# Optimization experiments

Measured on AMD Instinct MI355X. Metric: run time of the kernel, lower is better.

Reference implementation:

```python
import math
import jax, jax.numpy as jnp
import numpy as np

Bn, NA, NE = 16384, 15, 16
H, NH, DH = 256, 4, 64
DO, DA, DE = 30, 32, 32
NACT, BS = 6, 2048


def setup_inputs():
    key = jax.random.key(0)
    c = [0]
    def nxt():
        c[0] += 1
        return jax.random.fold_in(key, c[0])
    def nrm(shape, scale=1.0):
        return jax.random.normal(nxt(), shape, jnp.float32) * scale
    sH = 1.0 / math.sqrt(H)
    own_raw = nrm((Bn, 1, DO))
    ally_raw = nrm((Bn, NA, DA))
    enemy_raw = nrm((Bn, NE, DE))
    # zero-rows encode invisible entities (mask is derived from all-zero check)
    mA = jax.random.bernoulli(nxt(), 0.8, (Bn, NA)).at[:, 0].set(True)
    mE = jax.random.bernoulli(nxt(), 0.8, (Bn, NE)).at[:, 0].set(True)
    ally_raw = ally_raw * mA[..., None]
    enemy_raw = enemy_raw * mE[..., None]
    return dict(
        own_raw=own_raw, ally_raw=ally_raw, enemy_raw=enemy_raw,
        hidden_state=nrm((Bn, H), 0.1),
        W_own=nrm((H, DO), 1.0 / math.sqrt(DO)), b_own=jnp.zeros((H,)),
        W_ally=nrm((H, DA), 1.0 / math.sqrt(DA)), b_ally=jnp.zeros((H,)),
        W_enemy=nrm((H, DE), 1.0 / math.sqrt(DE)), b_enemy=jnp.zeros((H,)),
        gt_w=nrm((2,), 0.1), gt_b=jnp.zeros((2,)),
        attnA_W=nrm((4, H, H), sH), attnA_b=jnp.zeros((4, H)),
        attnE_W=nrm((4, H, H), sH), attnE_b=jnp.zeros((4, H)),
        clnA_W=nrm((2, H, H), 0.1 * sH), clnA_b=jnp.zeros((2, H)),
        clnE_W=nrm((2, H, H), 0.1 * sH), clnE_b=jnp.zeros((2, H)),
        ln3_g=jnp.ones((3 * H,)), ln3_b=jnp.zeros((3 * H,)),
        gru_Wih=nrm((3 * H, 3 * H), 1.0 / math.sqrt(3 * H)),
        gru_Whh=nrm((3 * H, H), sH),
        gru_bih=jnp.zeros((3 * H,)), gru_bhh=jnp.zeros((3 * H,)),
        Wv_head=nrm((1, H), sH), bv_head=jnp.zeros((1,)),
        Wtb=nrm((2, H), sH), btb=jnp.zeros((2,)),
        log_tau=jnp.zeros((2,)),
        Wmq=nrm((H, H), sH), bmq=jnp.zeros((H,)),
        prototypes=nrm((NACT, H), sH),
        Wqs=nrm((H, H), sH), bqs=jnp.zeros((H,)),
        Wke=nrm((H, H), sH), bke=jnp.zeros((H,)),
        bs=BS,
    )


def _group_temp(cnt, w, b):
    # GroupTemp: positive temperature from group cardinality
    return jax.nn.softplus(w * jnp.log1p(cnt) + b) + 1.0


def _mhga(q, K, mask, temp, W, b):
    # multi-head group attention: single query over a small entity set
    B, N, _ = K.shape
    qh = (q @ W[0].T + b[0]).reshape(B, NH, DH)
    kh = (K @ W[1].T + b[1]).reshape(B, N, NH, DH)
    vh = (K @ W[2].T + b[2]).reshape(B, N, NH, DH)
    s = jnp.einsum('bhd,bnhd->bhn', qh, kh) / math.sqrt(DH)
    s = s / temp[:, None, None]
    s = jnp.where(mask[:, None, :], s, -1e30)
    p = jax.nn.softmax(s, axis=-1)
    z = jnp.einsum('bhn,bnhd->bhd', p, vh).reshape(B, H)
    return z @ W[3].T + b[3]


def _cln(x, cond, W, b, eps=1e-5):
    # conditional LayerNorm: scale/shift predicted from own-feature embedding
    mu = x.mean(-1, keepdims=True)
    var = ((x - mu) ** 2).mean(-1, keepdims=True)
    xn = (x - mu) * jax.lax.rsqrt(var + eps)
    gamma = 1.0 + cond @ W[0].T + b[0]
    beta = cond @ W[1].T + b[1]
    return gamma * xn + beta


def _ln(x, g, b, eps=1e-5):
    mu = x.mean(-1, keepdims=True)
    var = ((x - mu) ** 2).mean(-1, keepdims=True)
    return (x - mu) * jax.lax.rsqrt(var + eps) * g + b


def reference(own_raw, ally_raw, enemy_raw, hidden_state, W_own, b_own,
              W_ally, b_ally, W_enemy, b_enemy, gt_w, gt_b,
              attnA_W, attnA_b, attnE_W, attnE_b,
              clnA_W, clnA_b, clnE_W, clnE_b, ln3_g, ln3_b,
              gru_Wih, gru_Whh, gru_bih, gru_bhh,
              Wv_head, bv_head, Wtb, btb, log_tau,
              Wmq, bmq, prototypes, Wqs, bqs, Wke, bke, bs):
    ally_mask = jnp.any(ally_raw != 0, axis=-1)     # [B,nA]
    enemy_mask = jnp.any(enemy_raw != 0, axis=-1)   # [B,nE]
    e_own = own_raw @ W_own.T + b_own               # [B,1,H]
    A = ally_raw @ W_ally.T + b_ally                # [B,nA,H]
    E = enemy_raw @ W_enemy.T + b_enemy             # [B,nE,H]
    q_src = e_own[:, 0]
    tA = _group_temp(ally_mask.sum(-1).astype(jnp.float32), gt_w[0], gt_b[0])
    tE = _group_temp(enemy_mask.sum(-1).astype(jnp.float32), gt_w[1], gt_b[1])
    zA = _cln(_mhga(q_src, A, ally_mask, tA, attnA_W, attnA_b), q_src, clnA_W, clnA_b)
    zE = _cln(_mhga(q_src, E, enemy_mask, tE, attnE_W, attnE_b), q_src, clnE_W, clnE_b)
    u = _ln(jnp.concatenate([q_src, zA, zE], axis=-1), ln3_g, ln3_b)
    # GRUCell (PyTorch gate layout: r, z, n)
    gi = u @ gru_Wih.T + gru_bih
    gh = hidden_state @ gru_Whh.T + gru_bhh
    ir, iz, inn = jnp.split(gi, 3, axis=-1)
    hr, hz, hn = jnp.split(gh, 3, axis=-1)
    r = jax.nn.sigmoid(ir + hr)
    zg = jax.nn.sigmoid(iz + hz)
    n = jnp.tanh(inn + r * hn)
    h = (1.0 - zg) * n + zg * hidden_state
    V = h @ Wv_head.T + bv_head                     # [B,1]
    tb = h @ Wtb.T + btb
    b_move, b_shoot = tb[:, 0:1], tb[:, 1:2]
    tau_move = jnp.exp(log_tau[0]) + 1e-6
    tau_shoot = jnp.exp(log_tau[1]) + 1e-6
    # prototype movement head
    q_mv = h @ Wmq.T + bmq
    A_move = q_mv @ prototypes.T / math.sqrt(H)
    A_move = A_move - A_move.mean(-1, keepdims=True)
    Q_move = V + b_move + A_move / tau_move
    # shoot pointer head over enemies
    q_sh = h @ Wqs.T + bqs
    Ke = E @ Wke.T + bke
    a = jnp.einsum('bh,bnh->bn', q_sh, Ke) / math.sqrt(H)
    emf = enemy_mask.astype(a.dtype)
    den = jnp.maximum(emf.sum(1, keepdims=True), 1.0)
    a = a - (a * emf).sum(1, keepdims=True) / den
    a = jnp.where(enemy_mask, a, -1e30)
    Q_shoot = V + b_shoot + a / tau_shoot
    Q = jnp.concatenate([Q_move, Q_shoot], axis=-1)[:, None, :]  # [B,1,NACT+nE]
    return Q, h.reshape(bs, -1, H)
```

## Files before the change

kernel.cpp:

```cpp
#include <hip/hip_runtime.h>
#include <math.h>

#define BN 16384

typedef float f32x4 __attribute__((ext_vector_type(4)));
typedef short bf16x8v __attribute__((ext_vector_type(8)));
typedef unsigned short u16x8 __attribute__((ext_vector_type(8)));
typedef unsigned short u16x4 __attribute__((ext_vector_type(4)));

static __device__ inline unsigned short f2bf(float f) {
  unsigned u = __float_as_uint(f);
  return (unsigned short)((u + 0x8000u) >> 16);
}
static __device__ inline float bf2f(unsigned short u) {
  return __uint_as_float(((unsigned)u) << 16);
}

#define WKA_OFF   0
#define WVA_OFF   8192
#define WKE_OFF   16384
#define WVE_OFF   24576
#define WKEF_OFF  32768
#define BKA_OFF   40960
#define BVA_OFF   41216
#define BKE_OFF   41472
#define BVE_OFF   41728
#define BKEF_OFF  41984
#define WMP_OFF   43008
#define BMP_OFF   44544
#define G_OFF     45056
#define BG_OFF    53248
#define WQB_OFF   53312
#define SC0_OFF   53568
#define BMG_OFF   53632
#define CLB_OFF   53888
#define BPJA_OFF  57088
#define BPJE_OFF  57344
#define BGRU_OFF  57600
#define BHD_OFF   16384

#define QSRC_OFF  65536
#define BUF1_OFF  (QSRC_OFF + BN*256)
#define BUF2_OFF  (BUF1_OFF + BN*256)
#define BUF3_OFF  (BUF2_OFF + BN*256)
#define BUF4_OFF  (BUF3_OFF + BN*256)
#define BUF5_OFF  (BUF4_OFF + BN*256)

#define GBUF_OFF  BUF1_OFF
#define AOUTA_OFF BUF3_OFF
#define AOUTE_OFF BUF4_OFF
#define GBB_OFF   BUF5_OFF
#define UB_OFF    (BUF5_OFF + 8388608)

#define HOFF      (BN*22)

#define MGB_S 0
#define CLA_S 65536
#define CLE_S 196608
#define PJA_S 327680
#define PJE_S 360448

__global__ __launch_bounds__(256) void k_fuseA(
    const float* __restrict__ attnA_W, const float* __restrict__ attnA_b,
    const float* __restrict__ attnE_W, const float* __restrict__ attnE_b,
    const float* __restrict__ W_ally,  const float* __restrict__ b_ally,
    const float* __restrict__ W_enemy, const float* __restrict__ b_enemy,
    const float* __restrict__ Wke,     const float* __restrict__ bke,
    const float* __restrict__ clnA_W,  const float* __restrict__ clnE_W,
    float* __restrict__ FW, unsigned short* __restrict__ WBc) {
  int g = blockIdx.x * 256 + threadIdx.x;
  if (g < 40960) {
    int m = g >> 13;
    int r = g & 8191;
    int d = r >> 5, j = r & 31;
    const float *Wout, *Win, *bin, *bout; float *dst, *dstb;
    switch (m) {
      case 0: Wout = attnA_W + 65536;  Win = W_ally;  bin = b_ally;  bout = attnA_b + 256; dst = FW + WKA_OFF;  dstb = FW + BKA_OFF;  break;
      case 1: Wout = attnA_W + 131072; Win = W_ally;  bin = b_ally;  bout = attnA_b + 512; dst = FW + WVA_OFF;  dstb = FW + BVA_OFF;  break;
      case 2: Wout = attnE_W + 65536;  Win = W_enemy; bin = b_enemy; bout = attnE_b + 256; dst = FW + WKE_OFF;  dstb = FW + BKE_OFF;  break;
      case 3: Wout = attnE_W + 131072; Win = W_enemy; bin = b_enemy; bout = attnE_b + 512; dst = FW + WVE_OFF;  dstb = FW + BVE_OFF;  break;
      default:Wout = Wke;              Win = W_enemy; bin = b_enemy; bout = bke;           dst = FW + WKEF_OFF; dstb = FW + BKEF_OFF; break;
    }
    float acc = 0.f;
    for (int c = 0; c < 256; ++c) acc += Wout[d*256 + c] * Win[c*32 + j];
    dst[d*32 + j] = acc;
    if (j == 0) {
      float b = bout[d];
      for (int c = 0; c < 256; ++c) b += Wout[d*256 + c] * bin[c];
      dstb[d] = b;
    }
  } else {
    int t = g - 40960;
    if (t < 65536) {
      int e = t * 4;
      const float* src = (e < 131072) ? clnA_W : clnE_W;
      int off = (e < 131072) ? 0 : 131072;
      float4 v = *(const float4*)(src + (e - off));
      u16x4 b; b.x = f2bf(v.x); b.y = f2bf(v.y); b.z = f2bf(v.z); b.w = f2bf(v.w);
      *(u16x4*)&WBc[CLA_S + e] = b;
    }
  }
}

__global__ __launch_bounds__(256) void k_fuseB(
    const float* __restrict__ protos, const float* __restrict__ Wmq,
    const float* __restrict__ bmq,    const float* __restrict__ Wqs,
    const float* __restrict__ bqs,
    const float* __restrict__ attnA_W, const float* __restrict__ attnA_b,
    const float* __restrict__ attnE_W, const float* __restrict__ attnE_b,
    const float* __restrict__ clnA_b,  const float* __restrict__ clnE_b,
    float* __restrict__ FW, unsigned short* __restrict__ WBc) {
  int g = blockIdx.x * 256 + threadIdx.x;
  const float* WKe_f = FW + WKEF_OFF;
  const float* bKe_f = FW + BKEF_OFF;
  if (g < 10240) {
    if (g < 1536) {
      int i = g >> 8, c = g & 255;
      float acc = 0.f;
      for (int d = 0; d < 256; ++d) acc += protos[i*256 + d] * Wmq[d*256 + c];
      FW[WMP_OFF + i*256 + c] = acc;
    } else if (g < 9728) {
      int r = g - 1536;
      int j = r >> 8, c = r & 255;
      float acc = 0.f;
      for (int d = 0; d < 256; ++d) acc += WKe_f[d*32 + j] * Wqs[d*256 + c];
      FW[G_OFF + j*256 + c] = acc;
    } else if (g < 9984) {
      int c = g - 9728;
      float acc = 0.f;
      for (int d = 0; d < 256; ++d) acc += Wqs[d*256 + c] * bKe_f[d];
      FW[WQB_OFF + c] = acc;
    } else if (g < 9990) {
      int i = g - 9984;
      float acc = 0.f;
      for (int d = 0; d < 256; ++d) acc += protos[i*256 + d] * bmq[d];
      FW[BMP_OFF + i] = acc;
    } else if (g < 10022) {
      int j = g - 9990;
      float acc = 0.f;
      for (int d = 0; d < 256; ++d) acc += WKe_f[d*32 + j] * bqs[d];
      FW[BG_OFF + j] = acc;
    } else if (g == 10022) {
      float acc = 0.f;
      for (int d = 0; d < 256; ++d) acc += bqs[d] * bKe_f[d];
      FW[SC0_OFF] = acc;
    }
  } else if (g < 77056) {
    int t = g - 10240;
    if (t < 65536) {
      int r = t >> 8, c = t & 255;
      int br = r >> 7, jj = r & 127, h = jj >> 5, jc = jj & 31;
      const float* W0 = br ? attnE_W : attnA_W;
      const float* Wk = FW + (br ? WKE_OFF : WKA_OFF);
      float acc = 0.f;
      for (int d = 0; d < 64; ++d)
        acc += W0[(h*64+d)*256 + c] * Wk[(h*64+d)*32 + jc];
      WBc[MGB_S + r*256 + c] = f2bf(acc);
    } else if (t < 65792) {
      int r = t - 65536;
      int br = r >> 7, jj = r & 127, h = jj >> 5, jc = jj & 31;
      const float* b0 = br ? attnE_b : attnA_b;
      const float* Wk = FW + (br ? WKE_OFF : WKA_OFF);
      float acc = 0.f;
      for (int d = 0; d < 64; ++d) acc += b0[h*64+d] * Wk[(h*64+d)*32 + jc];
      FW[BMG_OFF + r] = acc;
    } else {
      int c = t - 65792;
      FW[CLB_OFF + c] = (c < 512) ? clnA_b[c] : clnE_b[c - 512];
    }
  } else {
    int t = g - 77056;
    if (t < 65536) {
      int br = t >> 15;
      int r0 = t & 32767;
      int o = r0 >> 7, r = r0 & 127, h = r >> 5, j = r & 31;
      const float* Wp = (br ? attnE_W : attnA_W) + 196608;
      const float* Wv = FW + (br ? WVE_OFF : WVA_OFF);
      float acc = 0.f;
      for (int d = 0; d < 64; ++d)
        acc += Wp[o*256 + h*64 + d] * Wv[(h*64+d)*32 + j];
      WBc[(br ? PJE_S : PJA_S) + o*128 + r] = f2bf(acc);
    } else if (t < 66048) {
      int r0 = t - 65536;
      int br = r0 >> 8, c = r0 & 255;
      const float* Wp = (br ? attnE_W : attnA_W) + 196608;
      const float* bv = FW + (br ? BVE_OFF : BVA_OFF);
      const float* pb = (br ? attnE_b : attnA_b) + 768;
      float acc = pb[c];
      for (int d = 0; d < 256; ++d) acc += Wp[c*256 + d] * bv[d];
      FW[(br ? BPJE_OFF : BPJA_OFF) + c] = acc;
    }
  }
}

__global__ __launch_bounds__(256) void k_fuse4(
    const float* __restrict__ Wv_head, const float* __restrict__ bv_head,
    const float* __restrict__ Wtb, const float* __restrict__ btb,
    float* __restrict__ FW, unsigned short* __restrict__ WHD) {
  int g = blockIdx.x * 256 + threadIdx.x;
  if (g < 32768) {
    int r = g >> 8, c = g & 255;
    float v;
    if (r == 0)       v = Wv_head[c];
    else if (r == 1)  v = Wtb[c];
    else if (r == 2)  v = Wtb[256 + c];
    else if (r < 9)   v = FW[WMP_OFF + (r - 3) * 256 + c];
    else if (r < 41)  v = FW[G_OFF + (r - 9) * 256 + c];
    else if (r == 41) v = FW[WQB_OFF + c];
    else              v = 0.f;
    WHD[r * 256 + c] = f2bf(v);
  } else if (g < 32896) {
    int r = g - 32768;
    float v;
    if (r == 0)       v = bv_head[0];
    else if (r == 1)  v = btb[0];
    else if (r == 2)  v = btb[1];
    else if (r < 9)   v = FW[BMP_OFF + r - 3];
    else if (r < 41)  v = FW[BG_OFF + r - 9];
    else if (r == 41) v = FW[SC0_OFF];
    else              v = 0.f;
    FW[BHD_OFF + r] = v;
  }
}

__global__ __launch_bounds__(256) void k_gruw(
    const float* __restrict__ Wih, const float* __restrict__ Whh,
    const float* __restrict__ bih, const float* __restrict__ bhh,
    unsigned short* __restrict__ WG, float* __restrict__ BG) {
  int t = blockIdx.x * 256 + threadIdx.x;
  if (t < 262144) {
    int e4 = t * 4;
    int p = e4 >> 10, c = e4 & 1023;
    int X = p >> 8, df = (p >> 6) & 3, g = (p >> 4) & 3, i = p & 15;
    int d = X * 64 + df * 16 + i;
    float4 v;
    if (c < 768) {
      if (g == 3) v = make_float4(0.f, 0.f, 0.f, 0.f);
      else        v = *(const float4*)(Wih + (long)(g * 256 + d) * 768 + c);
    } else {
      int ch = c - 768;
      if (g == 2) v = make_float4(0.f, 0.f, 0.f, 0.f);
      else {
        int row = (g == 3 ? 512 : g * 256) + d;
        v = *(const float4*)(Whh + (long)row * 256 + ch);
      }
    }
    u16x4 b; b.x = f2bf(v.x); b.y = f2bf(v.y); b.z = f2bf(v.z); b.w = f2bf(v.w);
    *(u16x4*)&WG[e4] = b;
  } else if (t < 263168) {
    int p = t - 262144;
    int X = p >> 8, df = (p >> 6) & 3, g = (p >> 4) & 3, i = p & 15;
    int d = X * 64 + df * 16 + i;
    float v;
    if (g == 0)      v = bih[d] + bhh[d];
    else if (g == 1) v = bih[256 + d] + bhh[256 + d];
    else if (g == 2) v = bih[512 + d];
    else             v = bhh[512 + d];
    BG[p] = v;
  }
}

template<int K, int NOUT>
__global__ __launch_bounds__(256) void k_densek(
    const float* __restrict__ A, const float* __restrict__ W,
    const float* __restrict__ bias, unsigned short* __restrict__ Cb) {
  constexpr int KB = 32;
  __shared__ float As[64][36];
  const int tid = threadIdx.x;
  const int s0 = blockIdx.x * 64;
  const int o0 = blockIdx.y * 64;
  const int ox = (tid & 15) * 4;
  const int sy = (tid >> 4) * 4;
  float acc[4][4] = {};
  const float* Abase = A + (long)s0 * K;
  for (int idx = tid; idx < 64 * KB; idx += 256) {
    int s = idx >> 5, c = idx & 31;
    As[s][c] = (c < K) ? Abase[(long)s * K + c] : 0.f;
  }
  __syncthreads();
  for (int kk = 0; kk < KB; kk += 4) {
    float a4[4][4];
    #pragma unroll
    for (int sj = 0; sj < 4; ++sj)
      *(float4*)a4[sj] = *(const float4*)&As[sy + sj][kk];
    #pragma unroll
    for (int oi = 0; oi < 4; ++oi) {
      float w4[4];
      #pragma unroll
      for (int kx = 0; kx < 4; ++kx) {
        int k = kk + kx;
        w4[kx] = (k < K) ? W[(long)(o0 + ox + oi) * K + k] : 0.f;
      }
      #pragma unroll
      for (int sj = 0; sj < 4; ++sj)
        #pragma unroll
        for (int kx = 0; kx < 4; ++kx)
          acc[sj][oi] = fmaf(a4[sj][kx], w4[kx], acc[sj][oi]);
    }
  }
  #pragma unroll
  for (int sj = 0; sj < 4; ++sj) {
    u16x4 b4;
    b4.x = f2bf(acc[sj][0] + bias[o0 + ox + 0]);
    b4.y = f2bf(acc[sj][1] + bias[o0 + ox + 1]);
    b4.z = f2bf(acc[sj][2] + bias[o0 + ox + 2]);
    b4.w = f2bf(acc[sj][3] + bias[o0 + ox + 3]);
    *(u16x4*)&Cb[(long)(s0 + sy + sj) * NOUT + o0 + ox] = b4;
  }
}

#define MM_PROLOG(GDX)                                                        \
  __shared__ __align__(16) unsigned short As[4096];                           \
  __shared__ __align__(16) unsigned short Ws[4096];                           \
  const int tid = threadIdx.x;                                                \
  const int pid = blockIdx.y * (GDX) + blockIdx.x;                            \
  const int bx = (pid >> 3) % (GDX);                                          \
  const int by = ((pid >> 3) / (GDX)) * 8 + (pid & 7);                        \
  const long s0 = (long)by * 128;                                             \
  const int wv = tid >> 6, l = tid & 63;                                      \
  const int wm = (wv >> 1) * 64, wn = (wv & 1) * 64;                          \
  const int lr = l & 15, lk = l >> 4;                                         \
  const int wrow = tid >> 2;                                                  \
  const int wslot = tid & 3;                                                  \
  (void)wrow; (void)wslot;                                                    \
  f32x4 acc[4][4] = {};

#define MM_MFMA_STEP                                                          \
  {                                                                           \
    bf16x8v af[4], bw[4];                                                     \
    _Pragma("unroll")                                                         \
    for (int m = 0; m < 4; ++m) {                                             \
      const int r = wm + m * 16 + lr;                                         \
      af[m] = *(const bf16x8v*)&As[r * 32 + ((lk ^ (r & 3)) * 8)];            \
    }                                                                         \
    _Pragma("unroll")                                                         \
    for (int n = 0; n < 4; ++n) {                                             \
      const int r = wn + n * 16 + lr;                                         \
      bw[n] = *(const bf16x8v*)&Ws[r * 32 + ((lk ^ (r & 3)) * 8)];            \
    }                                                                         \
    _Pragma("unroll")                                                         \
    for (int m = 0; m < 4; ++m)                                               \
      _Pragma("unroll")                                                       \
      for (int n = 0; n < 4; ++n)                                             \
        acc[m][n] = __builtin_amdgcn_mfma_f32_16x16x32_bf16(af[m], bw[n], acc[m][n], 0, 0, 0); \
  }

__global__ __launch_bounds__(256) void k_mm_qs(
    const unsigned short* __restrict__ Abf, const unsigned short* __restrict__ W,
    const float* __restrict__ bias, float* __restrict__ Cg,
    unsigned short* __restrict__ Cgb) {
  MM_PROLOG(10)
  const int o0 = bx * 128;
  u16x8 pw[2], pa_b[2];
  const unsigned short* Wb = W + (long)o0 * 256;
  #pragma unroll
  for (int p = 0; p < 2; ++p) {
    const int r = wrow + 64 * p;
    pw[p]   = *(const u16x8*)(Wb + (long)r * 256 + wslot * 8);
    pa_b[p] = *(const u16x8*)(Abf + (s0 + r) * 256 + wslot * 8);
  }
  for (int ch = 0; ch < 8; ++ch) {
    if (ch) __syncthreads();
    #pragma unroll
    for (int p = 0; p < 2; ++p) {
      const int r = wrow + 64 * p;
      const int ps = (wslot ^ (r & 3)) * 8;
      *(u16x8*)&Ws[r * 32 + ps] = pw[p];
      *(u16x8*)&As[r * 32 + ps] = pa_b[p];
    }
    __syncthreads();
    if (ch + 1 < 8) {
      const int k0 = (ch + 1) * 32;
      #pragma unroll
      for (int p = 0; p < 2; ++p) {
        const int r = wrow + 64 * p;
        pw[p]   = *(const u16x8*)(Wb + (long)r * 256 + k0 + wslot * 8);
        pa_b[p] = *(const u16x8*)(Abf + (s0 + r) * 256 + k0 + wslot * 8);
      }
    }
    MM_MFMA_STEP
  }
  if (bx < 2) {
    const int ob = bx * 128;
    #pragma unroll
    for (int n = 0; n < 4; ++n) {
      const float b = bias[o0 + wn + n * 16 + lr];
      #pragma unroll
      for (int m = 0; m < 4; ++m) {
        const long rowb = s0 + wm + m * 16 + lk * 4;
        #pragma unroll
        for (int r = 0; r < 4; ++r)
          Cg[(rowb + r) * 256 + ob + wn + n * 16 + lr] = acc[m][n][r] + b;
      }
    }
  } else {
    const int ob = (bx - 2) * 128;
    #pragma unroll
    for (int n = 0; n < 4; ++n) {
      const float b = bias[o0 + wn + n * 16 + lr];
      #pragma unroll
      for (int m = 0; m < 4; ++m) {
        const long rowb = s0 + wm + m * 16 + lk * 4;
        #pragma unroll
        for (int r = 0; r < 4; ++r)
          Cgb[(rowb + r) * 1024 + ob + wn + n * 16 + lr] = f2bf(acc[m][n][r] + b);
      }
    }
  }
}

__global__ __launch_bounds__(256) void k_mm_pv(
    const unsigned short* __restrict__ pal, const unsigned short* __restrict__ W,
    const float* __restrict__ bias, float* __restrict__ CA, float* __restrict__ CE) {
  MM_PROLOG(4)
  const int o0 = bx * 128;
  const int br = bx >> 1;
  const unsigned short* Abf = pal + br * 128;
  u16x8 pw[2], pa_b[2];
  const unsigned short* Wb = W + (long)o0 * 128;
  #pragma unroll
  for (int p = 0; p < 2; ++p) {
    const int r = wrow + 64 * p;
    pw[p]   = *(const u16x8*)(Wb + (long)r * 128 + wslot * 8);
    pa_b[p] = *(const u16x8*)(Abf + (s0 + r) * 256 + wslot * 8);
  }
  for (int ch = 0; ch < 4; ++ch) {
    if (ch) __syncthreads();
    #pragma unroll
    for (int p = 0; p < 2; ++p) {
      const int r = wrow + 64 * p;
      const int ps = (wslot ^ (r & 3)) * 8;
      *(u16x8*)&Ws[r * 32 + ps] = pw[p];
      *(u16x8*)&As[r * 32 + ps] = pa_b[p];
    }
    __syncthreads();
    if (ch + 1 < 4) {
      const int k0 = (ch + 1) * 32;
      #pragma unroll
      for (int p = 0; p < 2; ++p) {
        const int r = wrow + 64 * p;
        pw[p]   = *(const u16x8*)(Wb + (long)r * 128 + k0 + wslot * 8);
        pa_b[p] = *(const u16x8*)(Abf + (s0 + r) * 256 + k0 + wslot * 8);
      }
    }
    MM_MFMA_STEP
  }
  float* C = br ? CE : CA;
  const int ob = (bx & 1) * 128;
  #pragma unroll
  for (int n = 0; n < 4; ++n) {
    const float b = bias[o0 + wn + n * 16 + lr];
    #pragma unroll
    for (int m = 0; m < 4; ++m) {
      const long rowb = s0 + wm + m * 16 + lk * 4;
      #pragma unroll
      for (int r = 0; r < 4; ++r)
        C[(rowb + r) * 256 + ob + wn + n * 16 + lr] = acc[m][n][r] + b;
    }
  }
}

__global__ __launch_bounds__(256, 4) void k_gru5(
    const unsigned short* __restrict__ UB, const float* __restrict__ hid,
    const unsigned short* __restrict__ WG, const float* __restrict__ BG,
    float* __restrict__ hout) {
  __shared__ __align__(16) unsigned short As[2048];
  __shared__ __align__(16) unsigned short Ws[8192];
  const int tid = threadIdx.x;
  const int pid = blockIdx.y * 4 + blockIdx.x;
  const int lin = pid >> 3;
  const int bx = lin & 3;
  const int by = (lin >> 2) * 8 + (pid & 7);
  const long s0 = (long)by * 64;
  const int wv = tid >> 6, l = tid & 63;
  const int wm = (wv >> 1) * 32;
  const int lr = l & 15, lk = l >> 4;
  const int row = tid >> 2;
  const int q = tid & 3;

  f32x4 acc[2][8] = {};
  u16x8 pw[4], pa_b;
  float4 pa_f[2];

  const unsigned short* Wb = WG + (long)(bx * 256) * 1024;

  #pragma unroll
  for (int p = 0; p < 4; ++p)
    pw[p] = *(const u16x8*)(Wb + (long)(row + 64 * p) * 1024 + q * 8);
  pa_b = *(const u16x8*)(UB + (s0 + row) * 768 + q * 8);

#define GRU5_MFMA(SKIPG)                                                      \
  {                                                                           \
    bf16x8v af[2], bw[8];                                                     \
    _Pragma("unroll")                                                         \
    for (int m = 0; m < 2; ++m) {                                             \
      const int r = wm + m * 16 + lr;                                         \
      af[m] = *(const bf16x8v*)&As[r * 32 + ((lk ^ (r & 3)) * 8)];            \
    }                                                                         \
    _Pragma("unroll")                                                         \
    for (int n = 0; n < 8; ++n) {                                             \
      const int r = (wv & 1) * 128 + n * 16 + lr;                             \
      bw[n] = *(const bf16x8v*)&Ws[r * 32 + ((lk ^ (r & 3)) * 8)];            \
    }                                                                         \
    _Pragma("unroll")                                                         \
    for (int m = 0; m < 2; ++m)                                               \
      _Pragma("unroll")                                                       \
      for (int n = 0; n < 8; ++n)                                             \
        if ((n & 3) != (SKIPG))                                               \
          acc[m][n] = __builtin_amdgcn_mfma_f32_16x16x32_bf16(af[m], bw[n], acc[m][n], 0, 0, 0); \
  }

  for (int ch = 0; ch < 24; ++ch) {
    if (ch) __syncthreads();
    #pragma unroll
    for (int p = 0; p < 4; ++p) {
      const int r = row + 64 * p;
      *(u16x8*)&Ws[r * 32 + ((q ^ (r & 3)) * 8)] = pw[p];
    }
    *(u16x8*)&As[row * 32 + ((q ^ (row & 3)) * 8)] = pa_b;
    __syncthreads();
    {
      const int k0 = (ch + 1) * 32;
      #pragma unroll
      for (int p = 0; p < 4; ++p)
        pw[p] = *(const u16x8*)(Wb + (long)(row + 64 * p) * 1024 + k0 + q * 8);
      if (ch + 1 < 24) {
        pa_b = *(const u16x8*)(UB + (s0 + row) * 768 + k0 + q * 8);
      } else {
        const float* Af = hid + (s0 + row) * 256 + q * 8;
        pa_f[0] = *(const float4*)(Af);
        pa_f[1] = *(const float4*)(Af + 4);
      }
    }
    GRU5_MFMA(3)
  }
  for (int ch = 24; ch < 32; ++ch) {
    __syncthreads();
    #pragma unroll
    for (int p = 0; p < 4; ++p) {
      const int r = row + 64 * p;
      *(u16x8*)&Ws[r * 32 + ((q ^ (r & 3)) * 8)] = pw[p];
    }
    {
      float fa[8];
      *(float4*)&fa[0] = pa_f[0];
      *(float4*)&fa[4] = pa_f[1];
      u16x8 pk;
      #pragma unroll
      for (int i = 0; i < 8; ++i) pk[i] = f2bf(fa[i]);
      *(u16x8*)&As[row * 32 + ((q ^ (row & 3)) * 8)] = pk;
    }
    __syncthreads();
    if (ch + 1 < 32) {
      const int k0 = (ch + 1) * 32;
      const int km = k0 - 768;
      #pragma unroll
      for (int p = 0; p < 4; ++p)
        pw[p] = *(const u16x8*)(Wb + (long)(row + 64 * p) * 1024 + k0 + q * 8);
      const float* Af = hid + (s0 + row) * 256 + km + q * 8;
      pa_f[0] = *(const float4*)(Af);
      pa_f[1] = *(const float4*)(Af + 4);
    }
    GRU5_MFMA(2)
  }

  #pragma unroll
  for (int df2 = 0; df2 < 2; ++df2) {
    const int df = (wv & 1) * 2 + df2;
    const int d = bx * 64 + df * 16 + lr;
    const int bb = bx * 256 + df * 64 + lr;
    const float bR = BG[bb], bZ = BG[bb + 16], bNi = BG[bb + 32], bNh = BG[bb + 48];
    #pragma unroll
    for (int m = 0; m < 2; ++m) {
      const long srow = s0 + wm + m * 16 + lk * 4;
      #pragma unroll
      for (int rr = 0; rr < 4; ++rr) {
        const long s = srow + rr;
        const float r_ = 1.f / (1.f + expf(-(acc[m][df2 * 4 + 0][rr] + bR)));
        const float z_ = 1.f / (1.f + expf(-(acc[m][df2 * 4 + 1][rr] + bZ)));
        const float n_ = tanhf(acc[m][df2 * 4 + 2][rr] + bNi +
                               r_ * (acc[m][df2 * 4 + 3][rr] + bNh));
        const float hp = hid[s * 256 + d];
        hout[s * 256 + d] = (1.f - z_) * n_ + z_ * hp;
      }
    }
  }
#undef GRU5_MFMA
}

__global__ __launch_bounds__(256) void k_core2(
    const float* __restrict__ rawA, const float* __restrict__ rawE,
    const float* __restrict__ g, const float* __restrict__ gt_w,
    const float* __restrict__ gt_b, unsigned short* __restrict__ pal) {
  __shared__ float A_[4][15][36];
  __shared__ float E_[4][16][36];
  __shared__ float G_[4][8][32];
  __shared__ float P_[4][8][16];
  const int tid = threadIdx.x;
  const int w = tid >> 6, l = tid & 63;
  const long s = (long)blockIdx.x * 4 + w;

  const float* ra = rawA + s * 480;
  const float* re = rawE + s * 512;
  const float* gr = g + s * 256;
  #pragma unroll
  for (int i = l; i < 120; i += 64) {
    float4 v = *(const float4*)(ra + i * 4);
    *(float4*)&A_[w][i >> 3][(i & 7) * 4] = v;
  }
  #pragma unroll
  for (int i = l; i < 128; i += 64) {
    float4 v = *(const float4*)(re + i * 4);
    *(float4*)&E_[w][i >> 3][(i & 7) * 4] = v;
  }
  {
    float4 v = *(const float4*)(gr + l * 4);
    *(float4*)&G_[w][l >> 3][(l & 7) * 4] = v;
  }
  __syncthreads();

  bool mv = false;
  if (l < 15) {
    #pragma unroll
    for (int c = 0; c < 8; ++c) {
      float4 x = *(const float4*)&A_[w][l][c * 4];
      mv |= (x.x != 0.f) | (x.y != 0.f) | (x.z != 0.f) | (x.w != 0.f);
    }
  } else if (l >= 16 && l < 32) {
    #pragma unroll
    for (int c = 0; c < 8; ++c) {
      float4 x = *(const float4*)&E_[w][l - 16][c * 4];
      mv |= (x.x != 0.f) | (x.y != 0.f) | (x.z != 0.f) | (x.w != 0.f);
    }
  }
  unsigned long long bal = __ballot(mv);
  unsigned mA = (unsigned)bal & 0x7FFFu;
  unsigned mE = (unsigned)(bal >> 16) & 0xFFFFu;
  float xa = gt_w[0] * log1pf((float)__popc(mA)) + gt_b[0];
  float spa = fmaxf(xa, 0.f) + log1pf(expf(-fabsf(xa)));
  float scaleA = 1.f / (8.f * (spa + 1.f));
  float xe = gt_w[1] * log1pf((float)__popc(mE)) + gt_b[1];
  float spe = fmaxf(xe, 0.f) + log1pf(expf(-fabsf(xe)));
  float scaleE = 1.f / (8.f * (spe + 1.f));

  {
    const int h = l >> 4, n = l & 15;
    const bool okA = (n < 15) && ((mA >> n) & 1);
    const bool okE = (mE >> n) & 1;
    const float* arow = &A_[w][n < 15 ? n : 0][0];
    const float* erow = &E_[w][n][0];
    const float* garow = &G_[w][h][0];
    const float* gerow = &G_[w][4 + h][0];
    float accA = 0.f, accE = 0.f;
    #pragma unroll
    for (int j = 0; j < 32; ++j) {
      accA = fmaf(garow[j], arow[j], accA);
      accE = fmaf(gerow[j], erow[j], accE);
    }
    float sA = okA ? accA * scaleA : -INFINITY;
    float sE = okE ? accE * scaleE : -INFINITY;
    float mAx = sA, mEx = sE;
    #pragma unroll
    for (int off = 8; off; off >>= 1) {
      mAx = fmaxf(mAx, __shfl_xor(mAx, off));
      mEx = fmaxf(mEx, __shfl_xor(mEx, off));
    }
    float eA = okA ? expf(sA - mAx) : 0.f;
    float eE = okE ? expf(sE - mEx) : 0.f;
    float suA = eA, suE = eE;
    #pragma unroll
    for (int off = 8; off; off >>= 1) {
      suA += __shfl_xor(suA, off);
      suE += __shfl_xor(suE, off);
    }
    P_[w][h][n] = eA / suA;
    P_[w][4 + h][n] = eE / suE;
  }
  __syncthreads();

  {
    const int j = l & 31, hh = l >> 5;
    unsigned short* po = pal + s * 256 + hh * 32 + j;
    #pragma unroll
    for (int r = 0; r < 2; ++r) {
      const int ha = r * 2 + hh;
      float a0 = 0.f, a1 = 0.f;
      #pragma unroll
      for (int n = 0; n < 15; ++n)
        a0 = fmaf(P_[w][ha][n], A_[w][n][j], a0);
      #pragma unroll
      for (int n = 0; n < 16; ++n)
        a1 = fmaf(P_[w][4 + ha][n], E_[w][n][j], a1);
      po[r * 64] = f2bf(a0);
      po[128 + r * 64] = f2bf(a1);
    }
  }
}

__global__ __launch_bounds__(256) void k_clnln(
    const float* __restrict__ aA, const float* __restrict__ aE,
    const unsigned short* __restrict__ qsb, const unsigned short* __restrict__ gbb,
    const float* __restrict__ g, const float* __restrict__ b,
    unsigned short* __restrict__ UB) {
  int w = threadIdx.x >> 6, l = threadIdx.x & 63;
  long s = (long)blockIdx.x * 4 + w;
  int d = l * 4;
  float4 vA = *(const float4*)(aA + s * 256 + d);
  float4 vE = *(const float4*)(aE + s * 256 + d);
  u16x4 qv = *(const u16x4*)(qsb + s * 256 + d);
  float4 vq = { bf2f(qv.x), bf2f(qv.y), bf2f(qv.z), bf2f(qv.w) };
  const unsigned short* gbr = gbb + s * 1024;
  float sumA = vA.x + vA.y + vA.z + vA.w;
  float ssqA = vA.x*vA.x + vA.y*vA.y + vA.z*vA.z + vA.w*vA.w;
  float sumE = vE.x + vE.y + vE.z + vE.w;
  float ssqE = vE.x*vE.x + vE.y*vE.y + vE.z*vE.z + vE.w*vE.w;
  #pragma unroll
  for (int off = 32; off > 0; off >>= 1) {
    sumA += __shfl_xor(sumA, off); ssqA += __shfl_xor(ssqA, off);
    sumE += __shfl_xor(sumE, off); ssqE += __shfl_xor(ssqE, off);
  }
  float muA = sumA * (1.f / 256.f);
  float rstdA = rsqrtf(ssqA * (1.f / 256.f) - muA * muA + 1e-5f);
  float muE = sumE * (1.f / 256.f);
  float rstdE = rsqrtf(ssqE * (1.f / 256.f) - muE * muE + 1e-5f);

  u16x4 u0 = *(const u16x4*)(gbr + d);
  u16x4 u1 = *(const u16x4*)(gbr + 256 + d);
  u16x4 u2 = *(const u16x4*)(gbr + 512 + d);
  u16x4 u3 = *(const u16x4*)(gbr + 768 + d);
  float4 gA4 = { bf2f(u0.x), bf2f(u0.y), bf2f(u0.z), bf2f(u0.w) };
  float4 bA4 = { bf2f(u1.x), bf2f(u1.y), bf2f(u1.z), bf2f(u1.w) };
  float4 gE4 = { bf2f(u2.x), bf2f(u2.y), bf2f(u2.z), bf2f(u2.w) };
  float4 bE4 = { bf2f(u3.x), bf2f(u3.y), bf2f(u3.z), bf2f(u3.w) };
  float4 zA, zE;
  zA.x = (1.f + gA4.x) * ((vA.x - muA) * rstdA) + bA4.x;
  zA.y = (1.f + gA4.y) * ((vA.y - muA) * rstdA) + bA4.y;
  zA.z = (1.f + gA4.z) * ((vA.z - muA) * rstdA) + bA4.z;
  zA.w = (1.f + gA4.w) * ((vA.w - muA) * rstdA) + bA4.w;
  zE.x = (1.f + gE4.x) * ((vE.x - muE) * rstdE) + bE4.x;
  zE.y = (1.f + gE4.y) * ((vE.y - muE) * rstdE) + bE4.y;
  zE.z = (1.f + gE4.z) * ((vE.z - muE) * rstdE) + bE4.z;
  zE.w = (1.f + gE4.w) * ((vE.w - muE) * rstdE) + bE4.w;

  float sum = vq.x+vq.y+vq.z+vq.w + zA.x+zA.y+zA.z+zA.w + zE.x+zE.y+zE.z+zE.w;
  float ssq = vq.x*vq.x+vq.y*vq.y+vq.z*vq.z+vq.w*vq.w
            + zA.x*zA.x+zA.y*zA.y+zA.z*zA.z+zA.w*zA.w
            + zE.x*zE.x+zE.y*zE.y+zE.z*zE.z+zE.w*zE.w;
  #pragma unroll
  for (int off = 32; off > 0; off >>= 1) {
    sum += __shfl_xor(sum, off); ssq += __shfl_xor(ssq, off);
  }
  float mu = sum * (1.f / 768.f);
  float rstd = rsqrtf(ssq * (1.f / 768.f) - mu * mu + 1e-5f);

  float4 g0 = *(const float4*)(g + d),       b0 = *(const float4*)(b + d);
  float4 g1 = *(const float4*)(g + 256 + d), b1 = *(const float4*)(b + 256 + d);
  float4 g2 = *(const float4*)(g + 512 + d), b2 = *(const float4*)(b + 512 + d);
  unsigned short* ur = UB + s * 768;
  u16x4 o;
  o.x = f2bf((vq.x - mu) * rstd * g0.x + b0.x);
  o.y = f2bf((vq.y - mu) * rstd * g0.y + b0.y);
  o.z = f2bf((vq.z - mu) * rstd * g0.z + b0.z);
  o.w = f2bf((vq.w - mu) * rstd * g0.w + b0.w);
  *(u16x4*)&ur[d] = o;
  o.x = f2bf((zA.x - mu) * rstd * g1.x + b1.x);
  o.y = f2bf((zA.y - mu) * rstd * g1.y + b1.y);
  o.z = f2bf((zA.z - mu) * rstd * g1.z + b1.z);
  o.w = f2bf((zA.w - mu) * rstd * g1.w + b1.w);
  *(u16x4*)&ur[256 + d] = o;
  o.x = f2bf((zE.x - mu) * rstd * g2.x + b2.x);
  o.y = f2bf((zE.y - mu) * rstd * g2.y + b2.y);
  o.z = f2bf((zE.z - mu) * rstd * g2.z + b2.z);
  o.w = f2bf((zE.w - mu) * rstd * g2.w + b2.w);
  *(u16x4*)&ur[512 + d] = o;
}

__global__ __launch_bounds__(256) void k_headsmm(
    const float* __restrict__ h, const unsigned short* __restrict__ WHD,
    const float* __restrict__ BHD, const float* __restrict__ eraw,
    const float* __restrict__ log_tau, float* __restrict__ Qout) {
  __shared__ __align__(16) unsigned short As[2048];
  __shared__ __align__(16) unsigned short Ws[2048];
  __shared__ float obs[64][49];
  const int tid = threadIdx.x;
  const long s0 = (long)blockIdx.x * 64;
  const int wv = tid >> 6, l = tid & 63;
  const int lr = l & 15, lk = l >> 4;
  const int row = tid >> 2;
  const int q = tid & 3;
  f32x4 acc[4] = {};
  u16x8 pw;
  float4 pa_f[2];
  pw = *(const u16x8*)(WHD + (long)row * 256 + q * 8);
  {
    const float* Af = h + (s0 + row) * 256 + q * 8;
    pa_f[0] = *(const float4*)(Af);
    pa_f[1] = *(const float4*)(Af + 4);
  }
  for (int ch = 0; ch < 8; ++ch) {
    if (ch) __syncthreads();
    *(u16x8*)&Ws[row * 32 + ((q ^ (row & 3)) * 8)] = pw;
    {
      float fa[8];
      *(float4*)&fa[0] = pa_f[0];
      *(float4*)&fa[4] = pa_f[1];
      u16x8 pk;
      #pragma unroll
      for (int i = 0; i < 8; ++i) pk[i] = f2bf(fa[i]);
      *(u16x8*)&As[row * 32 + ((q ^ (row & 3)) * 8)] = pk;
    }
    __syncthreads();
    if (ch + 1 < 8) {
      const int k0 = (ch + 1) * 32;
      pw = *(const u16x8*)(WHD + (long)row * 256 + k0 + q * 8);
      const float* Af = h + (s0 + row) * 256 + k0 + q * 8;
      pa_f[0] = *(const float4*)(Af);
      pa_f[1] = *(const float4*)(Af + 4);
    }
    {
      bf16x8v af, bw[4];
      {
        const int r = wv * 16 + lr;
        af = *(const bf16x8v*)&As[r * 32 + ((lk ^ (r & 3)) * 8)];
      }
      #pragma unroll
      for (int n = 0; n < 4; ++n) {
        const int r = n * 16 + lr;
        bw[n] = *(const bf16x8v*)&Ws[r * 32 + ((lk ^ (r & 3)) * 8)];
      }
      #pragma unroll
      for (int n = 0; n < 4; ++n)
        acc[n] = __builtin_amdgcn_mfma_f32_16x16x32_bf16(af, bw[n], acc[n], 0, 0, 0);
    }
  }
  #pragma unroll
  for (int n = 0; n < 3; ++n) {
    const int col = n * 16 + lr;
    const float b = BHD[col];
    const int rowo = wv * 16 + lk * 4;
    #pragma unroll
    for (int rr = 0; rr < 4; ++rr)
      obs[rowo + rr][col] = acc[n][rr] + b;
  }
  __syncthreads();
  const float itm = 1.f / (expf(log_tau[0]) + 1e-6f);
  const float its = 1.f / (expf(log_tau[1]) + 1e-6f);
  for (int rep = 0; rep < 4; ++rep) {
    const int sloc = rep * 16 + (tid >> 4);
    const int i = tid & 15;
    const long s = s0 + sloc;
    const float V = obs[sloc][0];
    const float* er = eraw + s * 512 + i * 32;
    bool valid = false; float a0 = 0.f;
    #pragma unroll
    for (int jb = 0; jb < 8; ++jb) {
      float4 e4 = *(const float4*)(er + jb * 4);
      valid |= (e4.x != 0.f) | (e4.y != 0.f) | (e4.z != 0.f) | (e4.w != 0.f);
      a0 += obs[sloc][9 + jb * 4 + 0] * e4.x + obs[sloc][9 + jb * 4 + 1] * e4.y +
            obs[sloc][9 + jb * 4 + 2] * e4.z + obs[sloc][9 + jb * 4 + 3] * e4.w;
    }
    float a = (a0 + obs[sloc][41]) * 0.0625f;
    float sa = valid ? a : 0.f;
    float cv = valid ? 1.f : 0.f;
    #pragma unroll
    for (int off = 8; off > 0; off >>= 1) {
      sa += __shfl_xor(sa, off);
      cv += __shfl_xor(cv, off);
    }
    float me = sa / fmaxf(cv, 1.f);
    Qout[s * 22 + 6 + i] = V + obs[sloc][2] + (valid ? (a - me) * its : -1e30f * its);
    if (i < 6) {
      float mean = 0.f;
      #pragma unroll
      for (int t = 0; t < 6; ++t) mean += obs[sloc][3 + t];
      mean *= (1.f / 6.f);
      Qout[s * 22 + i] = V + obs[sloc][1] + (obs[sloc][3 + i] - mean) * 0.0625f * itm;
    }
  }
}

extern "C" void kernel_launch(void* const* d_in, const int* in_sizes, int n_in,
                              void* d_out, int out_size, void* d_ws, size_t ws_size,
                              hipStream_t stream) {
  const float* own_raw   = (const float*)d_in[0];
  const float* ally_raw  = (const float*)d_in[1];
  const float* enemy_raw = (const float*)d_in[2];
  const float* hidden    = (const float*)d_in[3];
  const float* W_own     = (const float*)d_in[4];
  const float* b_own     = (const float*)d_in[5];
  const float* W_ally    = (const float*)d_in[6];
  const float* b_ally    = (const float*)d_in[7];
  const float* W_enemy   = (const float*)d_in[8];
  const float* b_enemy   = (const float*)d_in[9];
  const float* gt_w      = (const float*)d_in[10];
  const float* gt_b      = (const float*)d_in[11];
  const float* attnA_W   = (const float*)d_in[12];
  const float* attnA_b   = (const float*)d_in[13];
  const float* attnE_W   = (const float*)d_in[14];
  const float* attnE_b   = (const float*)d_in[15];
  const float* clnA_W    = (const float*)d_in[16];
  const float* clnA_b    = (const float*)d_in[17];
  const float* clnE_W    = (const float*)d_in[18];
  const float* clnE_b    = (const float*)d_in[19];
  const float* ln3_g     = (const float*)d_in[20];
  const float* ln3_b     = (const float*)d_in[21];
  const float* gru_Wih   = (const float*)d_in[22];
  const float* gru_Whh   = (const float*)d_in[23];
  const float* gru_bih   = (const float*)d_in[24];
  const float* gru_bhh   = (const float*)d_in[25];
  const float* Wv_head   = (const float*)d_in[26];
  const float* bv_head   = (const float*)d_in[27];
  const float* Wtb       = (const float*)d_in[28];
  const float* btb       = (const float*)d_in[29];
  const float* log_tau   = (const float*)d_in[30];
  const float* Wmq       = (const float*)d_in[31];
  const float* bmq       = (const float*)d_in[32];
  const float* protos    = (const float*)d_in[33];
  const float* Wqs       = (const float*)d_in[34];
  const float* bqs       = (const float*)d_in[35];
  const float* Wke       = (const float*)d_in[36];
  const float* bke       = (const float*)d_in[37];

  float* ws  = (float*)d_ws;
  float* out = (float*)d_out;
  float* hout = out + HOFF;
  unsigned short* WB   = (unsigned short*)hout;
  unsigned short* qsb  = (unsigned short*)(ws + BUF2_OFF);
  unsigned short* palb = (unsigned short*)(ws + QSRC_OFF);
  unsigned short* WHD  = (unsigned short*)ws;
  unsigned short* wgru = (unsigned short*)(ws + BUF1_OFF);
  unsigned short* gbb  = (unsigned short*)(ws + GBB_OFF);
  unsigned short* ub   = (unsigned short*)(ws + UB_OFF);

  k_fuseA<<<416, 256, 0, stream>>>(attnA_W, attnA_b, attnE_W, attnE_b,
                                   W_ally, b_ally, W_enemy, b_enemy, Wke, bke,
                                   clnA_W, clnE_W, ws, WB);
  k_fuseB<<<559, 256, 0, stream>>>(protos, Wmq, bmq, Wqs, bqs,
                                   attnA_W, attnA_b, attnE_W, attnE_b,
                                   clnA_b, clnE_b, ws, WB);
  k_fuse4<<<129, 256, 0, stream>>>(Wv_head, bv_head, Wtb, btb, ws, WHD);

  k_densek<30, 256><<<dim3(BN/64, 4), 256, 0, stream>>>(own_raw, W_own, b_own, qsb);

  k_mm_qs<<<dim3(10, 128), 256, 0, stream>>>(qsb, WB, ws + BMG_OFF,
                                             ws + GBUF_OFF, gbb);

  k_core2<<<BN/4, 256, 0, stream>>>(ally_raw, enemy_raw, ws + GBUF_OFF,
                                    gt_w, gt_b, palb);

  k_gruw<<<1028, 256, 0, stream>>>(gru_Wih, gru_Whh, gru_bih, gru_bhh,
                                   wgru, ws + BGRU_OFF);

  k_mm_pv<<<dim3(4, 128), 256, 0, stream>>>(palb, WB + PJA_S, ws + BPJA_OFF,
                                            ws + AOUTA_OFF, ws + AOUTE_OFF);

  k_clnln<<<BN/4, 256, 0, stream>>>(ws + AOUTA_OFF, ws + AOUTE_OFF, qsb, gbb,
                                    ln3_g, ln3_b, ub);

  k_gru5<<<dim3(4, 256), 256, 0, stream>>>(ub, hidden, wgru, ws + BGRU_OFF, hout);

  k_headsmm<<<BN/64, 256, 0, stream>>>(hout, WHD, ws + BHD_OFF, enemy_raw,
                                       log_tau, out);
}
```

Measured before the change: 196.5 us.

## Enlarge GRU GEMM tile to 128 rows with 512-thread blocks

The fused GRU GEMM kernel now processes 128 batch rows per block with 8 waves instead of 64 rows with 4 waves, halving the grid. Each wave owns a 64x64 output tile (4x4 MFMA accumulators), and each K-chunk of staged weights is reused across twice as many rows, cutting global weight traffic per output. The trade-off is fewer blocks, a larger LDS footprint and different register pressure, which may lower occupancy.

Measured after the change: 187.2 us. 4.7% less time.

```diff
diff --git a/kernel.cpp b/kernel.cpp
--- a/kernel.cpp
+++ b/kernel.cpp
@@ -460,70 +460,69 @@
   }
 }
 
-__global__ __launch_bounds__(256, 4) void k_gru5(
+__global__ __launch_bounds__(512, 4) void k_gru6(
     const unsigned short* __restrict__ UB, const float* __restrict__ hid,
     const unsigned short* __restrict__ WG, const float* __restrict__ BG,
     float* __restrict__ hout) {
-  __shared__ __align__(16) unsigned short As[2048];
+  __shared__ __align__(16) unsigned short As[4096];
   __shared__ __align__(16) unsigned short Ws[8192];
   const int tid = threadIdx.x;
   const int pid = blockIdx.y * 4 + blockIdx.x;
   const int lin = pid >> 3;
   const int bx = lin & 3;
   const int by = (lin >> 2) * 8 + (pid & 7);
-  const long s0 = (long)by * 64;
+  const long s0 = (long)by * 128;
   const int wv = tid >> 6, l = tid & 63;
-  const int wm = (wv >> 1) * 32;
+  const int sh = wv >> 2;
+  const int cq = wv & 3;
   const int lr = l & 15, lk = l >> 4;
   const int row = tid >> 2;
   const int q = tid & 3;
 
-  f32x4 acc[2][8] = {};
-  u16x8 pw[4], pa_b;
+  f32x4 acc[4][4] = {};
+  u16x8 pw[2], pa_b;
   float4 pa_f[2];
 
   const unsigned short* Wb = WG + (long)(bx * 256) * 1024;
 
-  #pragma unroll
-  for (int p = 0; p < 4; ++p)
-    pw[p] = *(const u16x8*)(Wb + (long)(row + 64 * p) * 1024 + q * 8);
+  pw[0] = *(const u16x8*)(Wb + (long)row * 1024 + q * 8);
+  pw[1] = *(const u16x8*)(Wb + (long)(row + 128) * 1024 + q * 8);
   pa_b = *(const u16x8*)(UB + (s0 + row) * 768 + q * 8);
 
-#define GRU5_MFMA(SKIPG)                                                      \
+#define GRU6_MFMA(SKIPG)                                                      \
   {                                                                           \
-    bf16x8v af[2], bw[8];                                                     \
+    bf16x8v af[4], bw[4];                                                     \
     _Pragma("unroll")                                                         \
-    for (int m = 0; m < 2; ++m) {                                             \
-      const int r = wm + m * 16 + lr;                                         \
+    for (int m = 0; m < 4; ++m) {                                             \
+      const int r = sh * 64 + m * 16 + lr;                                    \
       af[m] = *(const bf16x8v*)&As[r * 32 + ((lk ^ (r & 3)) * 8)];            \
     }                                                                         \
     _Pragma("unroll")                                                         \
-    for (int n = 0; n < 8; ++n) {                                             \
-      const int r = (wv & 1) * 128 + n * 16 + lr;                             \
+    for (int n = 0; n < 4; ++n) {                                             \
+      const int r = cq * 64 + n * 16 + lr;                                    \
       bw[n] = *(const bf16x8v*)&Ws[r * 32 + ((lk ^ (r & 3)) * 8)];            \
     }                                                                         \
     _Pragma("unroll")                                                         \
-    for (int m = 0; m < 2; ++m)                                               \
+    for (int m = 0; m < 4; ++m)                                               \
       _Pragma("unroll")                                                       \
-      for (int n = 0; n < 8; ++n)                                             \
-        if ((n & 3) != (SKIPG))                                               \
+      for (int n = 0; n < 4; ++n)                                             \
+        if (n != (SKIPG))                                                     \
           acc[m][n] = __builtin_amdgcn_mfma_f32_16x16x32_bf16(af[m], bw[n], acc[m][n], 0, 0, 0); \
   }
 
   for (int ch = 0; ch < 24; ++ch) {
     if (ch) __syncthreads();
-    #pragma unroll
-    for (int p = 0; p < 4; ++p) {
-      const int r = row + 64 * p;
-      *(u16x8*)&Ws[r * 32 + ((q ^ (r & 3)) * 8)] = pw[p];
-    }
-    *(u16x8*)&As[row * 32 + ((q ^ (row & 3)) * 8)] = pa_b;
+    {
+      *(u16x8*)&Ws[row * 32 + ((q ^ (row & 3)) * 8)] = pw[0];
+      const int r1 = row + 128;
+      *(u16x8*)&Ws[r1 * 32 + ((q ^ (r1 & 3)) * 8)] = pw[1];
+      *(u16x8*)&As[row * 32 + ((q ^ (row & 3)) * 8)] = pa_b;
+    }
     __syncthreads();
     {
       const int k0 = (ch + 1) * 32;
-      #pragma unroll
-      for (int p = 0; p < 4; ++p)
-        pw[p] = *(const u16x8*)(Wb + (long)(row + 64 * p) * 1024 + k0 + q * 8);
+      pw[0] = *(const u16x8*)(Wb + (long)row * 1024 + k0 + q * 8);
+      pw[1] = *(const u16x8*)(Wb + (long)(row + 128) * 1024 + k0 + q * 8);
       if (ch + 1 < 24) {
         pa_b = *(const u16x8*)(UB + (s0 + row) * 768 + k0 + q * 8);
       } else {
@@ -532,16 +531,14 @@
         pa_f[1] = *(const float4*)(Af + 4);
       }
     }
-    GRU5_MFMA(3)
+    GRU6_MFMA(3)
   }
   for (int ch = 24; ch < 32; ++ch) {
     __syncthreads();
-    #pragma unroll
-    for (int p = 0; p < 4; ++p) {
-      const int r = row + 64 * p;
-      *(u16x8*)&Ws[r * 32 + ((q ^ (r & 3)) * 8)] = pw[p];
-    }
     {
+      *(u16x8*)&Ws[row * 32 + ((q ^ (row & 3)) * 8)] = pw[0];
+      const int r1 = row + 128;
+      *(u16x8*)&Ws[r1 * 32 + ((q ^ (r1 & 3)) * 8)] = pw[1];
       float fa[8];
       *(float4*)&fa[0] = pa_f[0];
       *(float4*)&fa[4] = pa_f[1];
@@ -554,38 +551,35 @@
     if (ch + 1 < 32) {
       const int k0 = (ch + 1) * 32;
       const int km = k0 - 768;
-      #pragma unroll
-      for (int p = 0; p < 4; ++p)
-        pw[p] = *(const u16x8*)(Wb + (long)(row + 64 * p) * 1024 + k0 + q * 8);
+      pw[0] = *(const u16x8*)(Wb + (long)row * 1024 + k0 + q * 8);
+      pw[1] = *(const u16x8*)(Wb + (long)(row + 128) * 1024 + k0 + q * 8);
       const float* Af = hid + (s0 + row) * 256 + km + q * 8;
       pa_f[0] = *(const float4*)(Af);
       pa_f[1] = *(const float4*)(Af + 4);
     }
-    GRU5_MFMA(2)
-  }
-
+    GRU6_MFMA(2)
+  }
+
+  const int d = bx * 64 + cq * 16 + lr;
+  const int bb = bx * 256 + cq * 64 + lr;
+  const float bR  = BG[bb];
+  const float bZ  = BG[bb + 16];
+  const float bNi = BG[bb + 32];
+  const float bNh = BG[bb + 48];
   #pragma unroll
-  for (int df2 = 0; df2 < 2; ++df2) {
-    const int df = (wv & 1) * 2 + df2;
-    const int d = bx * 64 + df * 16 + lr;
-    const int bb = bx * 256 + df * 64 + lr;
-    const float bR = BG[bb], bZ = BG[bb + 16], bNi = BG[bb + 32], bNh = BG[bb + 48];
-    #pragma unroll
-    for (int m = 0; m < 2; ++m) {
-      const long srow = s0 + wm + m * 16 + lk * 4;
-      #pragma unroll
-      for (int rr = 0; rr < 4; ++rr) {
-        const long s = srow + rr;
-        const float r_ = 1.f / (1.f + expf(-(acc[m][df2 * 4 + 0][rr] + bR)));
-        const float z_ = 1.f / (1.f + expf(-(acc[m][df2 * 4 + 1][rr] + bZ)));
-        const float n_ = tanhf(acc[m][df2 * 4 + 2][rr] + bNi +
-                               r_ * (acc[m][df2 * 4 + 3][rr] + bNh));
-        const float hp = hid[s * 256 + d];
-        hout[s * 256 + d] = (1.f - z_) * n_ + z_ * hp;
-      }
-    }
-  }
-#undef GRU5_MFMA
+  for (int m = 0; m < 4; ++m) {
+    const long srow = s0 + sh * 64 + m * 16 + lk * 4;
+    #pragma unroll
+    for (int rr = 0; rr < 4; ++rr) {
+      const long s = srow + rr;
+      const float r_ = 1.f / (1.f + expf(-(acc[m][0][rr] + bR)));
+      const float z_ = 1.f / (1.f + expf(-(acc[m][1][rr] + bZ)));
+      const float n_ = tanhf(acc[m][2][rr] + bNi + r_ * (acc[m][3][rr] + bNh));
+      const float hp = hid[s * 256 + d];
+      hout[s * 256 + d] = (1.f - z_) * n_ + z_ * hp;
+    }
+  }
+#undef GRU6_MFMA
 }
 
 __global__ __launch_bounds__(256) void k_core2(
@@ -957,7 +951,7 @@
   k_clnln<<<BN/4, 256, 0, stream>>>(ws + AOUTA_OFF, ws + AOUTE_OFF, qsb, gbb,
                                     ln3_g, ln3_b, ub);
 
-  k_gru5<<<dim3(4, 256), 256, 0, stream>>>(ub, hidden, wgru, ws + BGRU_OFF, hout);
+  k_gru6<<<dim3(4, 128), 512, 0, stream>>>(ub, hidden, wgru, ws + BGRU_OFF, hout);
 
   k_headsmm<<<BN/64, 256, 0, stream>>>(hout, WHD, ws + BHD_OFF, enemy_raw,
                                        log_tau, out);
```
